# Optimization experiments

Measured on AMD Instinct MI355X. Metric: run time of the kernel, lower is better.

## Reference

```python
import jax, jax.numpy as jnp
import numpy as np

B, S, D, H, FF = 8, 1024, 2048, 16, 8192
Dh = D // H
EPS = 1e-5

def _layernorm(x, g, b):
    m = jnp.mean(x, axis=-1, keepdims=True)
    v = jnp.mean(jnp.square(x - m), axis=-1, keepdims=True)
    return (x - m) / jnp.sqrt(v + EPS) * g + b

def setup_inputs() -> dict:
    key = jax.random.key(0)
    ks = jax.random.split(key, 12)
    sc_d = 1.0 / np.sqrt(D)
    sc_ff = 1.0 / np.sqrt(FF)
    return {
        "x": jax.random.normal(ks[0], (B, S, D), dtype=jnp.float32),
        "mask": jnp.ones((S, S), dtype=jnp.int32),
        "Wq": jax.random.normal(ks[1], (D, D), dtype=jnp.float32) * sc_d,
        "bq": jnp.zeros((D,), dtype=jnp.float32),
        "Wk": jax.random.normal(ks[2], (D, D), dtype=jnp.float32) * sc_d,
        "bk": jnp.zeros((D,), dtype=jnp.float32),
        "Wv": jax.random.normal(ks[3], (D, D), dtype=jnp.float32) * sc_d,
        "bv": jnp.zeros((D,), dtype=jnp.float32),
        "Wo": jax.random.normal(ks[4], (D, D), dtype=jnp.float32) * sc_d,
        "bo": jnp.zeros((D,), dtype=jnp.float32),
        "W1": jax.random.normal(ks[5], (FF, D), dtype=jnp.float32) * sc_d,
        "b1": jnp.zeros((FF,), dtype=jnp.float32),
        "W2": jax.random.normal(ks[6], (D, FF), dtype=jnp.float32) * sc_ff,
        "b2": jnp.zeros((D,), dtype=jnp.float32),
        "g1": jnp.ones((D,), dtype=jnp.float32),
        "be1": jnp.zeros((D,), dtype=jnp.float32),
        "g2": jnp.ones((D,), dtype=jnp.float32),
        "be2": jnp.zeros((D,), dtype=jnp.float32),
    }

def reference(x, mask, Wq, bq, Wk, bk, Wv, bv, Wo, bo, W1, b1, W2, b2, g1, be1, g2, be2):
    # --- multi-head attention (chunk along d_model == reshape to heads) ---
    q = (x @ Wq.T + bq).reshape(B, S, H, Dh)
    k = (x @ Wk.T + bk).reshape(B, S, H, Dh)
    v = (x @ Wv.T + bv).reshape(B, S, H, Dh)
    score = jnp.einsum('bqhd,bkhd->bhqk', q, k) / jnp.sqrt(jnp.float32(Dh))
    score = jnp.where(mask == 0, jnp.float32(-1e9), score)
    attn = jax.nn.softmax(score, axis=-1)
    out = jnp.einsum('bhqk,bkhd->bqhd', attn, v).reshape(B, S, D)
    attn_out = out @ Wo.T + bo
    # --- residual + post-LN ---
    x1 = _layernorm(attn_out + x, g1, be1)
    # --- FFN ---
    h = jax.nn.relu(x1 @ W1.T + b1)
    ffn_out = h @ W2.T + b2
    return _layernorm(ffn_out + x1, g2, be2)
```

## Files before the change

### kernel.cpp

```cpp
#include <hip/hip_runtime.h>
#include <cstdint>
#include <cstddef>


typedef unsigned short u16;
typedef unsigned int   u32;
typedef unsigned long long u64;
typedef __attribute__((ext_vector_type(8))) short short8;
typedef __attribute__((ext_vector_type(4))) float f32x4;

constexpr int Bc  = 8;
constexpr int Sc  = 1024;
constexpr int Dc  = 2048;
constexpr int Hc  = 16;
constexpr int Dhc = 128;
constexpr int FFc = 8192;
constexpr int Mc  = Bc * Sc;

__device__ __forceinline__ u16 f2b(float f) {
  u32 u = __builtin_bit_cast(u32, f);
  u += 0x7fffu + ((u >> 16) & 1u);
  return (u16)(u >> 16);
}
__device__ __forceinline__ u32 pack2(float a, float b) {
  return (u32)f2b(a) | ((u32)f2b(b) << 16);
}
__device__ __forceinline__ void unpack8(uint4 u, float* f) {
  u32 w[4] = {u.x, u.y, u.z, u.w};
#pragma unroll
  for (int i = 0; i < 4; ++i) {
    f[2 * i + 0] = __builtin_bit_cast(float, w[i] << 16);
    f[2 * i + 1] = __builtin_bit_cast(float, w[i] & 0xffff0000u);
  }
}

#define GLOAD_LDS16(gp, lp)                                                    \
  __builtin_amdgcn_global_load_lds(                                            \
      (const __attribute__((address_space(1))) void*)(gp),                     \
      (__attribute__((address_space(3))) void*)(lp), 16, 0, 0)

__global__ __launch_bounds__(256) void cvt_f32_bf16(const float* __restrict__ in,
                                                    u16* __restrict__ out, int n) {
  int i = (blockIdx.x * 256 + threadIdx.x) << 2;
  if (i >= n) return;
  float4 v = *(const float4*)(in + i);
  ushort4 o;
  o.x = f2b(v.x); o.y = f2b(v.y); o.z = f2b(v.z); o.w = f2b(v.w);
  *(ushort4*)(out + i) = o;
}

__global__ __launch_bounds__(256) void mask_bits(const int* __restrict__ mask,
                                                 u64* __restrict__ mb) {
  int t = blockIdx.x * 256 + threadIdx.x;
  int r = t >> 4, wd = t & 15;
  const int* p = mask + (size_t)r * Sc + wd * 64;
  u64 bits = 0;
#pragma unroll 16
  for (int i = 0; i < 64; i += 4) {
    int4 q = *(const int4*)(p + i);
    bits |= (u64)(q.x != 0) << (i + 0);
    bits |= (u64)(q.y != 0) << (i + 1);
    bits |= (u64)(q.z != 0) << (i + 2);
    bits |= (u64)(q.w != 0) << (i + 3);
  }
  mb[t] = bits;
}

template <int MODE>
__global__ __launch_bounds__(512, 2) void gemm256tb(const u16* __restrict__ A,
                                                    const u16* __restrict__ Bt,
                                                    const float* __restrict__ bias,
                                                    const float* __restrict__ bias2,
                                                    const float* __restrict__ bias3,
                                                    u16* __restrict__ C,
                                                    int M, int N, int K) {
  __shared__ u16 Abuf[4][256 * 32];
  __shared__ u16 Bbuf[4][256 * 32];

  const int nbn = N >> 8;
  const int nwg = (M >> 8) * nbn;
  int bid = blockIdx.x;
  int sw = (bid & 7) * (nwg >> 3) + (bid >> 3);
  const int m0 = (sw / nbn) << 8;
  const int n0 = (sw % nbn) << 8;

  const int tid  = threadIdx.x;
  const int lane = tid & 63;
  const int w    = tid >> 6;
  const int wm   = w >> 2;
  const int wn   = w & 3;

  const int rowA = lane & 15;
  const int g4   = lane >> 4;

  const int p16  = lane << 4;
  const int wsw  = p16 ^ (((p16 >> 9) & 1) << 5);
  const int s_rr = wsw >> 6;
  const int s_cc = (wsw & 63) >> 1;

  const int sb = (rowA * 64 + g4 * 16) ^ (((rowA >> 3) & 1) << 5);

  const int NT = K >> 5;

  const u16* aP = A  + (size_t)(m0 + w * 32 + s_rr) * K + s_cc;
  const u16* bP = Bt + (size_t)(n0 + w * 32 + s_rr) * K + s_cc;
  const size_t rstep = (size_t)16 * K;

  auto stage = [&](int tt, const u16* ap, const u16* bp) {
    int buf = tt & 3;
    GLOAD_LDS16(ap,         &Abuf[buf][(2 * w + 0) * 512]);
    GLOAD_LDS16(ap + rstep, &Abuf[buf][(2 * w + 1) * 512]);
    GLOAD_LDS16(bp,         &Bbuf[buf][(2 * w + 0) * 512]);
    GLOAD_LDS16(bp + rstep, &Bbuf[buf][(2 * w + 1) * 512]);
  };

  auto readF = [&](int tt, short8* aF, short8* bF) {
    int buf = tt & 3;
#pragma unroll
    for (int n = 0; n < 4; ++n)
      bF[n] = *(const short8*)((const char*)&Bbuf[buf][(wn * 4 + n) * 512] + sb);
#pragma unroll
    for (int i = 0; i < 8; ++i)
      aF[i] = *(const short8*)((const char*)&Abuf[buf][(wm * 8 + i) * 512] + sb);
  };

  f32x4 acc[8][4];
#pragma unroll
  for (int m = 0; m < 8; ++m)
#pragma unroll
    for (int n = 0; n < 4; ++n) acc[m][n] = (f32x4){0.f, 0.f, 0.f, 0.f};

  stage(0, aP, bP);
  stage(1, aP + 32, bP + 32);
  stage(2, aP + 64, bP + 64);
  aP += 96; bP += 96;
  asm volatile("s_waitcnt vmcnt(4)" ::: "memory");
  __builtin_amdgcn_s_barrier();

  short8 a0[8], b0[4], a1[8], b1[4];
  readF(0, a0, b0);

  auto body = [&](int t, short8* aC, short8* bC, short8* aN, short8* bN) {
    if (t + 1 < NT) readF(t + 1, aN, bN);
    if (t + 3 < NT) { stage(t + 3, aP, bP); aP += 32; bP += 32; }
    __builtin_amdgcn_s_setprio(1);
#pragma unroll
    for (int i = 0; i < 8; ++i)
#pragma unroll
      for (int n = 0; n < 4; ++n)
        acc[i][n] = __builtin_amdgcn_mfma_f32_16x16x32_bf16(aC[i], bC[n], acc[i][n], 0, 0, 0);
    __builtin_amdgcn_s_setprio(0);
    if (t + 3 < NT) { asm volatile("s_waitcnt vmcnt(4)" ::: "memory"); }
    else            { asm volatile("s_waitcnt vmcnt(0)" ::: "memory"); }
    __builtin_amdgcn_s_barrier();
  };

  for (int t = 0; t < NT; t += 2) {
    body(t,     a0, b0, a1, b1);
    body(t + 1, a1, b1, a0, b0);
  }

  const int ci = lane & 15;
  const int ri = g4 << 2;

  if (MODE == 3) {
    const int cb   = n0 + wn * 64;
    const int seg  = cb >> 11;
    const int cseg = cb & 2047;
    const float* bp_ = (seg == 0) ? bias : (seg == 1) ? bias2 : bias3;
    float bvv[4];
#pragma unroll
    for (int n = 0; n < 4; ++n) bvv[n] = bp_[cseg + n * 16 + ci];
    if (seg < 2) {
      u16* Cs = C + (size_t)seg * Mc * Dc;
#pragma unroll
      for (int m = 0; m < 8; ++m) {
        int row0 = m0 + wm * 128 + m * 16 + ri;
#pragma unroll
        for (int j = 0; j < 4; ++j) {
          u16* cp = Cs + (size_t)(row0 + j) * Dc + cseg + ci;
#pragma unroll
          for (int n = 0; n < 4; ++n)
            cp[n * 16] = f2b(acc[m][n][j] + bvv[n]);
        }
      }
    } else {
      u16* Cv = C + (size_t)2 * Mc * Dc;
#pragma unroll
      for (int n = 0; n < 4; ++n) {
        int col = cseg + n * 16 + ci;
#pragma unroll
        for (int m = 0; m < 8; ++m) {
          int row0 = m0 + wm * 128 + m * 16 + ri;
          ushort4 pk;
          pk.x = f2b(acc[m][n][0] + bvv[n]);
          pk.y = f2b(acc[m][n][1] + bvv[n]);
          pk.z = f2b(acc[m][n][2] + bvv[n]);
          pk.w = f2b(acc[m][n][3] + bvv[n]);
          size_t addr = ((size_t)((row0 >> 10) * Hc + (col >> 7)) * 128 + (col & 127)) * 1024
                        + (row0 & 1023);
          *(ushort4*)(Cv + addr) = pk;
        }
      }
    }
  } else {
    float bvv[4];
#pragma unroll
    for (int n = 0; n < 4; ++n) bvv[n] = bias[n0 + wn * 64 + n * 16 + ci];
#pragma unroll
    for (int m = 0; m < 8; ++m) {
      int row0 = m0 + wm * 128 + m * 16 + ri;
#pragma unroll
      for (int j = 0; j < 4; ++j) {
        u16* cp = C + (size_t)(row0 + j) * N + n0 + wn * 64 + ci;
#pragma unroll
        for (int n = 0; n < 4; ++n) {
          float v = acc[m][n][j] + bvv[n];
          if (MODE == 1) v = fmaxf(v, 0.f);
          cp[n * 16] = f2b(v);
        }
      }
    }
  }
}

__global__ __launch_bounds__(256, 2) void attn_mfma(
    const u16* __restrict__ qb,
    const u16* __restrict__ kb,
    const u16* __restrict__ vt,
    const u64* __restrict__ mb,
    u16* __restrict__ ob)
{
  __shared__ u16 Ks[64 * 128];
  __shared__ u16 Vts[128 * 64];
  __shared__ u16 Ps[4][32 * 64];

  const int bid = blockIdx.x;
  const int l   = (bid & 7) * 128 + (bid >> 3);
  const int qt  = l & 7;
  const int bh  = l >> 3;
  const int h   = bh & (Hc - 1);
  const int b   = bh >> 4;
  const int q0  = qt * 128;

  const int tid  = threadIdx.x;
  const int lane = tid & 63;
  const int w    = tid >> 6;
  const int rowA = lane & 15;
  const int g4   = lane >> 4;
  const int kq16 = g4 << 3;
  const int ri   = g4 << 2;

  const size_t tokbase = (size_t)b * Sc * Dc + (size_t)h * Dhc;
  const size_t vtbase  = (size_t)bh * 128 * 1024;
  const int qwbase = q0 + w * 32;

  short8 qf[2][4];
#pragma unroll
  for (int m = 0; m < 2; ++m)
#pragma unroll
    for (int kk = 0; kk < 4; ++kk)
      qf[m][kk] = *reinterpret_cast<const short8*>(
          qb + tokbase + (size_t)(qwbase + m * 16 + rowA) * Dc + kk * 32 + kq16);

  f32x4 O[2][8];
#pragma unroll
  for (int m = 0; m < 2; ++m)
#pragma unroll
    for (int n = 0; n < 8; ++n) O[m][n] = (f32x4){0.f, 0.f, 0.f, 0.f};
  float mrow[2][4], lrow[2][4];
#pragma unroll
  for (int m = 0; m < 2; ++m)
#pragma unroll
    for (int j = 0; j < 4; ++j) { mrow[m][j] = -INFINITY; lrow[m][j] = 0.f; }

  const float scale = 0.08838834764831845f;

  for (int kt = 0; kt < Sc / 64; ++kt) {
    const int k0 = kt * 64;
    __syncthreads();
#pragma unroll
    for (int i = 0; i < 4; ++i) {
      int chunk = w * 4 + i;
      int gb = (chunk * 64 + lane) * 16;
      int L  = gb ^ (((gb >> 8) & 7) << 4);
      int row = L >> 8, ce = (L & 255) >> 1;
      GLOAD_LDS16(kb + tokbase + (size_t)(k0 + row) * Dc + ce, &Ks[chunk * 512]);
    }
#pragma unroll
    for (int i = 0; i < 4; ++i) {
      int chunk = w * 4 + i;
      int gb = (chunk * 64 + lane) * 16;
      int L  = gb ^ (((gb >> 7) & 7) << 4);
      int row = L >> 7, ce = (L & 127) >> 1;
      GLOAD_LDS16(vt + vtbase + (size_t)row * 1024 + k0 + ce, &Vts[chunk * 512]);
    }
    __syncthreads();

    f32x4 s[2][4];
#pragma unroll
    for (int m = 0; m < 2; ++m)
#pragma unroll
      for (int n = 0; n < 4; ++n) s[m][n] = (f32x4){0.f, 0.f, 0.f, 0.f};
#pragma unroll
    for (int kk = 0; kk < 4; ++kk) {
      short8 bfk[4];
#pragma unroll
      for (int n = 0; n < 4; ++n) {
        int krow = n * 16 + rowA;
        int by = (krow * 256 + kk * 64 + (g4 << 4)) ^ ((krow & 7) << 4);
        bfk[n] = *reinterpret_cast<const short8*>((const char*)Ks + by);
      }
#pragma unroll
      for (int m = 0; m < 2; ++m)
#pragma unroll
        for (int n = 0; n < 4; ++n)
          s[m][n] = __builtin_amdgcn_mfma_f32_16x16x32_bf16(qf[m][kk], bfk[n], s[m][n], 0, 0, 0);
    }

    float alpha[2][4];
#pragma unroll
    for (int m = 0; m < 2; ++m) {
      u64 wb_[4];
#pragma unroll
      for (int j = 0; j < 4; ++j)
        wb_[j] = mb[(size_t)(qwbase + m * 16 + ri + j) * 16 + kt];
#pragma unroll
      for (int j = 0; j < 4; ++j) {
        float pv[4];
        float mx = -3.0e38f;
#pragma unroll
        for (int n = 0; n < 4; ++n) {
          float x = s[m][n][j] * scale;
          if (!((wb_[j] >> (n * 16 + rowA)) & 1)) x = -1e9f;
          pv[n] = x;
          mx = fmaxf(mx, x);
        }
        mx = fmaxf(mx, __shfl_xor(mx, 1));
        mx = fmaxf(mx, __shfl_xor(mx, 2));
        mx = fmaxf(mx, __shfl_xor(mx, 4));
        mx = fmaxf(mx, __shfl_xor(mx, 8));
        float mnew = fmaxf(mrow[m][j], mx);
        float a = __expf(mrow[m][j] - mnew);
        mrow[m][j] = mnew;
        alpha[m][j] = a;
        float rs = 0.f;
#pragma unroll
        for (int n = 0; n < 4; ++n) {
          float p = __expf(pv[n] - mnew);
          pv[n] = p;
          rs += p;
        }
        rs += __shfl_xor(rs, 1);
        rs += __shfl_xor(rs, 2);
        rs += __shfl_xor(rs, 4);
        rs += __shfl_xor(rs, 8);
        lrow[m][j] = lrow[m][j] * a + rs;
        int prow = m * 16 + ri + j;
#pragma unroll
        for (int n = 0; n < 4; ++n) {
          int by = (prow * 128 + 2 * (n * 16 + rowA)) ^ ((prow & 7) << 4);
          *(u16*)((char*)Ps[w] + by) = f2b(pv[n]);
        }
      }
    }
    asm volatile("s_waitcnt lgkmcnt(0)" ::: "memory");

#pragma unroll
    for (int m = 0; m < 2; ++m)
#pragma unroll
      for (int n = 0; n < 8; ++n)
#pragma unroll
        for (int j = 0; j < 4; ++j) O[m][n][j] *= alpha[m][j];

    short8 pa[2][2];
#pragma unroll
    for (int m = 0; m < 2; ++m)
#pragma unroll
      for (int kk = 0; kk < 2; ++kk) {
        int prow = m * 16 + rowA;
        int by = (prow * 128 + kk * 64 + (g4 << 4)) ^ ((prow & 7) << 4);
        pa[m][kk] = *reinterpret_cast<const short8*>((const char*)Ps[w] + by);
      }
#pragma unroll
    for (int kk = 0; kk < 2; ++kk)
#pragma unroll
      for (int n = 0; n < 8; ++n) {
        int drow = n * 16 + rowA;
        int by = (drow * 128 + kk * 64 + (g4 << 4)) ^ ((drow & 7) << 4);
        short8 bfv = *reinterpret_cast<const short8*>((const char*)Vts + by);
#pragma unroll
        for (int m = 0; m < 2; ++m)
          O[m][n] = __builtin_amdgcn_mfma_f32_16x16x32_bf16(pa[m][kk], bfv, O[m][n], 0, 0, 0);
      }
  }

  float inv[2][4];
#pragma unroll
  for (int m = 0; m < 2; ++m)
#pragma unroll
    for (int j = 0; j < 4; ++j) inv[m][j] = 1.f / lrow[m][j];
#pragma unroll
  for (int m = 0; m < 2; ++m)
#pragma unroll
    for (int n = 0; n < 8; ++n) {
      int dcol = n * 16 + rowA;
#pragma unroll
      for (int j = 0; j < 4; ++j) {
        int qg = qwbase + m * 16 + ri + j;
        ob[tokbase + (size_t)qg * Dc + dcol] = f2b(O[m][n][j] * inv[m][j]);
      }
    }
}

template <int RES_BF16, int OUT_BF16>
__global__ __launch_bounds__(256) void ln_kernel(const u16* __restrict__ a,
                                                 const void* __restrict__ resid,
                                                 const float* __restrict__ g,
                                                 const float* __restrict__ be,
                                                 void* __restrict__ out) {
  int row = blockIdx.x;
  int tid = threadIdx.x;
  int c0  = tid << 3;

  float v[8], vr[8];
  uint4 ua = *(const uint4*)(a + (size_t)row * Dc + c0);
  unpack8(ua, v);
  if (RES_BF16) {
    uint4 ur = *(const uint4*)((const u16*)resid + (size_t)row * Dc + c0);
    unpack8(ur, vr);
  } else {
    const float* rp = (const float*)resid + (size_t)row * Dc + c0;
    float4 f0 = *(const float4*)rp;
    float4 f1 = *(const float4*)(rp + 4);
    vr[0] = f0.x; vr[1] = f0.y; vr[2] = f0.z; vr[3] = f0.w;
    vr[4] = f1.x; vr[5] = f1.y; vr[6] = f1.z; vr[7] = f1.w;
  }

  float s = 0.f, ss = 0.f;
#pragma unroll
  for (int j = 0; j < 8; ++j) {
    v[j] += vr[j];
    s += v[j];
    ss += v[j] * v[j];
  }
#pragma unroll
  for (int off = 32; off; off >>= 1) {
    s  += __shfl_down(s, off);
    ss += __shfl_down(ss, off);
  }
  __shared__ float rs[4], rss[4], stat[2];
  if ((tid & 63) == 0) { rs[tid >> 6] = s; rss[tid >> 6] = ss; }
  __syncthreads();
  if (tid == 0) {
    float t  = rs[0] + rs[1] + rs[2] + rs[3];
    float tt = rss[0] + rss[1] + rss[2] + rss[3];
    float mean = t * (1.f / Dc);
    float var  = tt * (1.f / Dc) - mean * mean;
    stat[0] = mean;
    stat[1] = rsqrtf(var + 1e-5f);
  }
  __syncthreads();
  float mean = stat[0], rstd = stat[1];

  float y[8];
#pragma unroll
  for (int j = 0; j < 8; ++j) y[j] = (v[j] - mean) * rstd * g[c0 + j] + be[c0 + j];

  if (OUT_BF16) {
    uint4 o;
    o.x = pack2(y[0], y[1]); o.y = pack2(y[2], y[3]);
    o.z = pack2(y[4], y[5]); o.w = pack2(y[6], y[7]);
    *(uint4*)((u16*)out + (size_t)row * Dc + c0) = o;
  } else {
    float* op = (float*)out + (size_t)row * Dc + c0;
    *(float4*)op       = (float4){y[0], y[1], y[2], y[3]};
    *(float4*)(op + 4) = (float4){y[4], y[5], y[6], y[7]};
  }
}

extern "C" void kernel_launch(void* const* d_in, const int* in_sizes, int n_in,
                              void* d_out, int out_size, void* d_ws, size_t ws_size,
                              hipStream_t stream) {
  (void)in_sizes; (void)n_in; (void)out_size; (void)ws_size;

  const float* x   = (const float*)d_in[0];
  const int*   mk  = (const int*)d_in[1];
  const float* Wq  = (const float*)d_in[2];
  const float* bq  = (const float*)d_in[3];
  const float* Wk  = (const float*)d_in[4];
  const float* bk  = (const float*)d_in[5];
  const float* Wv  = (const float*)d_in[6];
  const float* bv  = (const float*)d_in[7];
  const float* Wo  = (const float*)d_in[8];
  const float* bo  = (const float*)d_in[9];
  const float* W1  = (const float*)d_in[10];
  const float* b1  = (const float*)d_in[11];
  const float* W2  = (const float*)d_in[12];
  const float* b2  = (const float*)d_in[13];
  const float* g1  = (const float*)d_in[14];
  const float* be1 = (const float*)d_in[15];
  const float* g2  = (const float*)d_in[16];
  const float* be2 = (const float*)d_in[17];
  float* outp = (float*)d_out;

  const size_t R = 16777216;
  u16* xb   = (u16*)d_ws;
  u16* wqkv = xb + R;
  u64* mbt  = (u64*)(wqkv + 13 * 1024 * 1024);
  u16* qb   = xb + 2 * R;
  u16* ao   = xb + 5 * R;
  u16* wst6 = xb + 6 * R;
  u16* x1   = xb + 6 * R;
  u16* ap   = xb + 7 * R;
  u16* w1s  = xb;
  u16* hb   = xb + 2 * R;
  u16* w2s  = xb + 7 * R;
  u16* ffn  = wqkv;

  const size_t MD = (size_t)Mc * Dc;

  auto cvt = [&](const float* src, u16* dst, int n) {
    cvt_f32_bf16<<<dim3((n + 1023) / 1024), dim3(256), 0, stream>>>(src, dst, n);
  };

  cvt(x, xb, Mc * Dc);
  cvt(Wq, wqkv,               Dc * Dc);
  cvt(Wk, wqkv + Dc * Dc,     Dc * Dc);
  cvt(Wv, wqkv + 2 * Dc * Dc, Dc * Dc);

  gemm256tb<3><<<dim3(32 * 24), dim3(512), 0, stream>>>(xb, wqkv, bq, bk, bv,
                                                        qb, Mc, 3 * Dc, Dc);

  mask_bits<<<dim3(64), dim3(256), 0, stream>>>(mk, mbt);

  attn_mfma<<<dim3(Bc * Hc * (Sc / 128)), dim3(256), 0, stream>>>(
      qb, qb + MD, qb + 2 * MD, mbt, ao);

  cvt(Wo, wst6, Dc * Dc);
  gemm256tb<0><<<dim3(32 * 8), dim3(512), 0, stream>>>(ao, wst6, bo, bo, bo,
                                                       ap, Mc, Dc, Dc);
  ln_kernel<0, 1><<<dim3(Mc), dim3(256), 0, stream>>>(ap, x, g1, be1, x1);

  cvt(W1, w1s, FFc * Dc);
  gemm256tb<1><<<dim3(32 * 32), dim3(512), 0, stream>>>(x1, w1s, b1, b1, b1,
                                                        hb, Mc, FFc, Dc);
  cvt(W2, w2s, Dc * FFc);
  gemm256tb<0><<<dim3(32 * 8), dim3(512), 0, stream>>>(hb, w2s, b2, b2, b2,
                                                       ffn, Mc, Dc, FFc);
  ln_kernel<1, 0><<<dim3(Mc), dim3(256), 0, stream>>>(ffn, x1, g2, be2, outp);
}
```

Measured before the change: 1.050 ms.

## Fuse residual add into GEMM epilogue and skip attention rescale when max barely grows

The output-projection and FFN2 GEMMs gain a MODE 4 epilogue that adds a bf16 residual before storing, so the layernorm kernels no longer read a separate residual tensor. The first residual now comes from the bf16 copy of x instead of fp32 x, which costs some precision. The attention kernel uses a lazy online-softmax rescale: O and l are rescaled only when some row's max grows by more than 8, which cuts exp and multiply work per tile. Buffer aliases are reshuffled so the residual buffers stay live while they are read.

Result: no change. 1.064 ms (+1.3%).

```diff
diff --git a/kernel.cpp b/kernel.cpp
--- a/kernel.cpp
+++ b/kernel.cpp
@@ -21,6 +21,9 @@
   u32 u = __builtin_bit_cast(u32, f);
   u += 0x7fffu + ((u >> 16) & 1u);
   return (u16)(u >> 16);
+}
+__device__ __forceinline__ float b2f(u16 r) {
+  return __builtin_bit_cast(float, (u32)r << 16);
 }
 __device__ __forceinline__ u32 pack2(float a, float b) {
   return (u32)f2b(a) | ((u32)f2b(b) << 16);
@@ -72,6 +75,7 @@
                                                     const float* __restrict__ bias,
                                                     const float* __restrict__ bias2,
                                                     const float* __restrict__ bias3,
+                                                    const u16* __restrict__ resid,
                                                     u16* __restrict__ C,
                                                     int M, int N, int K) {
   __shared__ u16 Abuf[4][256 * 32];
@@ -212,12 +216,20 @@
       int row0 = m0 + wm * 128 + m * 16 + ri;
 #pragma unroll
       for (int j = 0; j < 4; ++j) {
-        u16* cp = C + (size_t)(row0 + j) * N + n0 + wn * 64 + ci;
-#pragma unroll
-        for (int n = 0; n < 4; ++n) {
-          float v = acc[m][n][j] + bvv[n];
-          if (MODE == 1) v = fmaxf(v, 0.f);
-          cp[n * 16] = f2b(v);
+        size_t roff = (size_t)(row0 + j) * N + n0 + wn * 64 + ci;
+        u16* cp = C + roff;
+        if (MODE == 4) {
+          const u16* rp = resid + roff;
+#pragma unroll
+          for (int n = 0; n < 4; ++n)
+            cp[n * 16] = f2b(acc[m][n][j] + bvv[n] + b2f(rp[n * 16]));
+        } else {
+#pragma unroll
+          for (int n = 0; n < 4; ++n) {
+            float v = acc[m][n][j] + bvv[n];
+            if (MODE == 1) v = fmaxf(v, 0.f);
+            cp[n * 16] = f2b(v);
+          }
         }
       }
     }
@@ -318,7 +330,7 @@
           s[m][n] = __builtin_amdgcn_mfma_f32_16x16x32_bf16(qf[m][kk], bfk[n], s[m][n], 0, 0, 0);
     }
 
-    float alpha[2][4];
+    float mx[2][4];
 #pragma unroll
     for (int m = 0; m < 2; ++m) {
       u64 wb_[4];
@@ -327,51 +339,66 @@
         wb_[j] = mb[(size_t)(qwbase + m * 16 + ri + j) * 16 + kt];
 #pragma unroll
       for (int j = 0; j < 4; ++j) {
-        float pv[4];
-        float mx = -3.0e38f;
+        float mj = -3.0e38f;
 #pragma unroll
         for (int n = 0; n < 4; ++n) {
           float x = s[m][n][j] * scale;
           if (!((wb_[j] >> (n * 16 + rowA)) & 1)) x = -1e9f;
-          pv[n] = x;
-          mx = fmaxf(mx, x);
+          s[m][n][j] = x;
+          mj = fmaxf(mj, x);
         }
-        mx = fmaxf(mx, __shfl_xor(mx, 1));
-        mx = fmaxf(mx, __shfl_xor(mx, 2));
-        mx = fmaxf(mx, __shfl_xor(mx, 4));
-        mx = fmaxf(mx, __shfl_xor(mx, 8));
-        float mnew = fmaxf(mrow[m][j], mx);
-        float a = __expf(mrow[m][j] - mnew);
-        mrow[m][j] = mnew;
-        alpha[m][j] = a;
-        float rs = 0.f;
+        mj = fmaxf(mj, __shfl_xor(mj, 1));
+        mj = fmaxf(mj, __shfl_xor(mj, 2));
+        mj = fmaxf(mj, __shfl_xor(mj, 4));
+        mj = fmaxf(mj, __shfl_xor(mj, 8));
+        mx[m][j] = mj;
+      }
+    }
+
+    float worst = -3.0e38f;
+#pragma unroll
+    for (int m = 0; m < 2; ++m)
+#pragma unroll
+      for (int j = 0; j < 4; ++j) worst = fmaxf(worst, mx[m][j] - mrow[m][j]);
+    if (__any(worst > 8.f)) {
+      float alpha[2][4];
+#pragma unroll
+      for (int m = 0; m < 2; ++m)
+#pragma unroll
+        for (int j = 0; j < 4; ++j) {
+          float mnew = fmaxf(mrow[m][j], mx[m][j]);
+          alpha[m][j] = __expf(mrow[m][j] - mnew);
+          mrow[m][j] = mnew;
+          lrow[m][j] *= alpha[m][j];
+        }
+#pragma unroll
+      for (int m = 0; m < 2; ++m)
+#pragma unroll
+        for (int n = 0; n < 8; ++n)
+#pragma unroll
+          for (int j = 0; j < 4; ++j) O[m][n][j] *= alpha[m][j];
+    }
+
+#pragma unroll
+    for (int m = 0; m < 2; ++m)
+#pragma unroll
+      for (int j = 0; j < 4; ++j) {
+        float rs_ = 0.f;
+        int prow = m * 16 + ri + j;
 #pragma unroll
         for (int n = 0; n < 4; ++n) {
-          float p = __expf(pv[n] - mnew);
-          pv[n] = p;
-          rs += p;
+          float p = __expf(s[m][n][j] - mrow[m][j]);
+          rs_ += p;
+          int by = (prow * 128 + 2 * (n * 16 + rowA)) ^ ((prow & 7) << 4);
+          *(u16*)((char*)Ps[w] + by) = f2b(p);
         }
-        rs += __shfl_xor(rs, 1);
-        rs += __shfl_xor(rs, 2);
-        rs += __shfl_xor(rs, 4);
-        rs += __shfl_xor(rs, 8);
-        lrow[m][j] = lrow[m][j] * a + rs;
-        int prow = m * 16 + ri + j;
-#pragma unroll
-        for (int n = 0; n < 4; ++n) {
-          int by = (prow * 128 + 2 * (n * 16 + rowA)) ^ ((prow & 7) << 4);
-          *(u16*)((char*)Ps[w] + by) = f2b(pv[n]);
-        }
-      }
-    }
+        rs_ += __shfl_xor(rs_, 1);
+        rs_ += __shfl_xor(rs_, 2);
+        rs_ += __shfl_xor(rs_, 4);
+        rs_ += __shfl_xor(rs_, 8);
+        lrow[m][j] += rs_;
+      }
     asm volatile("s_waitcnt lgkmcnt(0)" ::: "memory");
-
-#pragma unroll
-    for (int m = 0; m < 2; ++m)
-#pragma unroll
-      for (int n = 0; n < 8; ++n)
-#pragma unroll
-        for (int j = 0; j < 4; ++j) O[m][n][j] *= alpha[m][j];
 
     short8 pa[2][2];
 #pragma unroll
@@ -413,9 +440,8 @@
     }
 }
 
-template <int RES_BF16, int OUT_BF16>
+template <int OUT_BF16>
 __global__ __launch_bounds__(256) void ln_kernel(const u16* __restrict__ a,
-                                                 const void* __restrict__ resid,
                                                  const float* __restrict__ g,
                                                  const float* __restrict__ be,
                                                  void* __restrict__ out) {
@@ -423,24 +449,13 @@
   int tid = threadIdx.x;
   int c0  = tid << 3;
 
-  float v[8], vr[8];
+  float v[8];
   uint4 ua = *(const uint4*)(a + (size_t)row * Dc + c0);
   unpack8(ua, v);
-  if (RES_BF16) {
-    uint4 ur = *(const uint4*)((const u16*)resid + (size_t)row * Dc + c0);
-    unpack8(ur, vr);
-  } else {
-    const float* rp = (const float*)resid + (size_t)row * Dc + c0;
-    float4 f0 = *(const float4*)rp;
-    float4 f1 = *(const float4*)(rp + 4);
-    vr[0] = f0.x; vr[1] = f0.y; vr[2] = f0.z; vr[3] = f0.w;
-    vr[4] = f1.x; vr[5] = f1.y; vr[6] = f1.z; vr[7] = f1.w;
-  }
 
   float s = 0.f, ss = 0.f;
 #pragma unroll
   for (int j = 0; j < 8; ++j) {
-    v[j] += vr[j];
     s += v[j];
     ss += v[j] * v[j];
   }
@@ -513,10 +528,10 @@
   u16* wst6 = xb + 6 * R;
   u16* x1   = xb + 6 * R;
   u16* ap   = xb + 7 * R;
-  u16* w1s  = xb;
+  u16* w1s  = wqkv;
   u16* hb   = xb + 2 * R;
   u16* w2s  = xb + 7 * R;
-  u16* ffn  = wqkv;
+  u16* ffn  = xb;
 
   const size_t MD = (size_t)Mc * Dc;
 
@@ -530,7 +545,7 @@
   cvt(Wv, wqkv + 2 * Dc * Dc, Dc * Dc);
 
   gemm256tb<3><<<dim3(32 * 24), dim3(512), 0, stream>>>(xb, wqkv, bq, bk, bv,
-                                                        qb, Mc, 3 * Dc, Dc);
+                                                        nullptr, qb, Mc, 3 * Dc, Dc);
 
   mask_bits<<<dim3(64), dim3(256), 0, stream>>>(mk, mbt);
 
@@ -538,15 +553,15 @@
       qb, qb + MD, qb + 2 * MD, mbt, ao);
 
   cvt(Wo, wst6, Dc * Dc);
-  gemm256tb<0><<<dim3(32 * 8), dim3(512), 0, stream>>>(ao, wst6, bo, bo, bo,
-                                                       ap, Mc, Dc, Dc);
-  ln_kernel<0, 1><<<dim3(Mc), dim3(256), 0, stream>>>(ap, x, g1, be1, x1);
+  gemm256tb<4><<<dim3(32 * 8), dim3(512), 0, stream>>>(ao, wst6, bo, bo, bo,
+                                                       xb, ap, Mc, Dc, Dc);
+  ln_kernel<1><<<dim3(Mc), dim3(256), 0, stream>>>(ap, g1, be1, x1);
 
   cvt(W1, w1s, FFc * Dc);
   gemm256tb<1><<<dim3(32 * 32), dim3(512), 0, stream>>>(x1, w1s, b1, b1, b1,
-                                                        hb, Mc, FFc, Dc);
+                                                        nullptr, hb, Mc, FFc, Dc);
   cvt(W2, w2s, Dc * FFc);
-  gemm256tb<0><<<dim3(32 * 8), dim3(512), 0, stream>>>(hb, w2s, b2, b2, b2,
-                                                       ffn, Mc, Dc, FFc);
-  ln_kernel<1, 0><<<dim3(Mc), dim3(256), 0, stream>>>(ffn, x1, g2, be2, outp);
-}
+  gemm256tb<4><<<dim3(32 * 8), dim3(512), 0, stream>>>(hb, w2s, b2, b2, b2,
+                                                       x1, ffn, Mc, Dc, FFc);
+  ln_kernel<0><<<dim3(Mc), dim3(256), 0, stream>>>(ffn, g2, be2, outp);
+}
```
